# Kernel optimization log

Measured on AMD Instinct MI355X. Metric: run time of the kernel, lower is better.

The kernel has to match this reference:

```python
import jax, jax.numpy as jnp
import numpy as np

LVALS = [0, 1, 2]
IN_MULT = 128
OUT_MULT = 128
NREPS = len(LVALS)                      # 3 irreps
DIM = sum(2 * l + 1 for l in LVALS)     # 9 = 1 + 3 + 5
BATCH = 65536


def setup_inputs() -> dict:
    key = jax.random.key(0)
    k1, k2, k3 = jax.random.split(key, 3)
    f = jax.random.normal(k1, (BATCH, IN_MULT, DIM), dtype=jnp.float32)
    # xavier_uniform over (nreps*out_mult, in_mult): fan_out = nreps*out_mult, fan_in = in_mult
    limit = float(np.sqrt(6.0 / (IN_MULT + NREPS * OUT_MULT)))
    weight = jax.random.uniform(k2, (NREPS * OUT_MULT, IN_MULT), minval=-limit, maxval=limit, dtype=jnp.float32)
    bias = jax.random.normal(k3, (OUT_MULT, 1), dtype=jnp.float32) * 0.01
    # per-dim irrep index: [0, 1,1,1, 2,2,2,2,2]
    indices = jnp.asarray(np.repeat(np.arange(NREPS), [2 * l + 1 for l in LVALS]), dtype=jnp.int32)
    scalar_locs = jnp.asarray([0], dtype=jnp.int32)  # degree-0 column(s)
    return {"f": f, "weight": weight, "bias": bias, "indices": indices, "scalar_locs": scalar_locs}


def reference(f, weight, bias, indices, scalar_locs):
    # Torch does (weight @ f) -> (..., nreps*out_mult, dim), views to
    # (..., nreps, out_mult, dim), then gathers along the nreps axis with the
    # per-dim irrep index. Equivalently: use the per-dim weight slice directly,
    # avoiding the nreps-expanded intermediate.
    w3 = weight.reshape(NREPS, OUT_MULT, IN_MULT)
    wd = w3[indices]                              # (DIM, OUT_MULT, IN_MULT)
    out = jnp.einsum('dnm,bmd->bnd', wd, f)       # (B, OUT_MULT, DIM)
    # bias (+ identity activation) on scalar (degree-0) columns only
    scal = out[..., scalar_locs] + bias           # (B, OUT_MULT, nscalar)
    out = out.at[..., scalar_locs].set(scal)
    return out
```

## Files before the change

kernel.cpp:

```cpp
#include <hip/hip_runtime.h>


#define IN_MULT   128
#define OUT_MULT  128
#define DIM       9
#define TB        16
#define TPB       8
#define THREADS   256
#define ROWSTRIDE 136
#define NROWS     144

typedef __attribute__((ext_vector_type(8))) short short8;
typedef __attribute__((ext_vector_type(4))) float f32x4;

__device__ __forceinline__ unsigned short f2bf(float x) {
    unsigned u = __builtin_bit_cast(unsigned, x);
    u += 0x7FFFu + ((u >> 16) & 1u);
    return (unsigned short)(u >> 16);
}

__global__ __launch_bounds__(THREADS, 2)
void eqlin_kernel(const float* __restrict__ f,
                  const float* __restrict__ weight,
                  const float* __restrict__ bias,
                  float* __restrict__ out) {
    __shared__ unsigned short smem[NROWS * ROWSTRIDE];

    const int tid  = threadIdx.x;
    const int lane = tid & 63;
    const int wv   = tid >> 6;
    const int quad = lane >> 4;
    const int l16  = lane & 15;

    short8 bfrag[3][2][4];
    #pragma unroll
    for (int g = 0; g < 3; ++g)
        #pragma unroll
        for (int nf = 0; nf < 2; ++nf)
            #pragma unroll
            for (int kk = 0; kk < 4; ++kk) {
                const float* wp = weight
                    + (size_t)(g * OUT_MULT + wv * 32 + nf * 16 + l16) * IN_MULT
                    + kk * 32 + quad * 8;
                float4 u0 = *(const float4*)wp;
                float4 u1 = *(const float4*)(wp + 4);
                short8 bb;
                bb[0] = (short)f2bf(u0.x); bb[1] = (short)f2bf(u0.y);
                bb[2] = (short)f2bf(u0.z); bb[3] = (short)f2bf(u0.w);
                bb[4] = (short)f2bf(u1.x); bb[5] = (short)f2bf(u1.y);
                bb[6] = (short)f2bf(u1.z); bb[7] = (short)f2bf(u1.w);
                bfrag[g][nf][kk] = bb;
            }

    float biasv[2];
    #pragma unroll
    for (int nf = 0; nf < 2; ++nf)
        biasv[nf] = bias[wv * 32 + nf * 16 + l16];

    for (int it = 0; it < TPB; ++it) {
        const int b0 = (blockIdx.x * TPB + it) * TB;
        const float* ftile = f + (size_t)b0 * (IN_MULT * DIM);

        __syncthreads();

        #pragma unroll
        for (int rr = 0; rr < 18; rr += 6) {
            float4 v[6];
            #pragma unroll
            for (int q = 0; q < 6; ++q)
                v[q] = *(const float4*)(ftile + 4 * (tid + THREADS * (rr + q)));
            #pragma unroll
            for (int q = 0; q < 6; ++q) {
                const int F0  = 4 * (tid + THREADS * (rr + q));
                const int bl  = F0 / 1152;
                const int rem = F0 - bl * 1152;
                const int m0  = rem / 9;
                const int d0  = rem - m0 * 9;
                float vals[4] = {v[q].x, v[q].y, v[q].z, v[q].w};
                #pragma unroll
                for (int j = 0; j < 4; ++j) {
                    int dd = d0 + j, mm = m0;
                    if (dd >= 9) { dd -= 9; mm += 1; }
                    int row;
                    if (dd == 0)      row = bl;
                    else if (dd < 4)  row = 16 + bl * 3 + (dd - 1);
                    else              row = 64 + bl * 5 + (dd - 4);
                    smem[row * ROWSTRIDE + mm] = f2bf(vals[j]);
                }
            }
        }

        __syncthreads();

        #pragma unroll
        for (int mf = 0; mf < 9; ++mf) {
            const int g = (mf == 0) ? 0 : (mf < 4 ? 1 : 2);
            short8 a[4];
            #pragma unroll
            for (int kk = 0; kk < 4; ++kk)
                a[kk] = *(const short8*)&smem[(mf * 16 + l16) * ROWSTRIDE + kk * 32 + quad * 8];
            #pragma unroll
            for (int nf = 0; nf < 2; ++nf) {
                f32x4 acc = {0.f, 0.f, 0.f, 0.f};
                #pragma unroll
                for (int kk = 0; kk < 4; ++kk)
                    acc = __builtin_amdgcn_mfma_f32_16x16x32_bf16(a[kk], bfrag[g][nf][kk], acc, 0, 0, 0);
                if (g == 0) {
                    acc[0] += biasv[nf]; acc[1] += biasv[nf];
                    acc[2] += biasv[nf]; acc[3] += biasv[nf];
                }
                const int n = wv * 32 + nf * 16 + l16;
                #pragma unroll
                for (int reg = 0; reg < 4; ++reg) {
                    const int row = mf * 16 + quad * 4 + reg;
                    int bl, d;
                    if (mf == 0)      { bl = row; d = 0; }
                    else if (mf < 4)  { int r = row - 16; bl = r / 3; d = 1 + (r - 3 * bl); }
                    else              { int r = row - 64; bl = r / 5; d = 4 + (r - 5 * bl); }
                    out[(size_t)(b0 + bl) * (OUT_MULT * DIM) + n * DIM + d] = acc[reg];
                }
            }
        }
    }
}

extern "C" void kernel_launch(void* const* d_in, const int* in_sizes, int n_in,
                              void* d_out, int out_size, void* d_ws, size_t ws_size,
                              hipStream_t stream) {
    (void)n_in; (void)out_size; (void)d_ws; (void)ws_size;
    const float* f  = (const float*)d_in[0];
    const float* w  = (const float*)d_in[1];
    const float* bi = (const float*)d_in[2];
    float* out = (float*)d_out;

    const int batch   = in_sizes[0] / (IN_MULT * DIM);
    const int nblocks = batch / (TB * TPB);
    eqlin_kernel<<<nblocks, THREADS, 0, stream>>>(f, w, bi, out);
}
```

Before: 737.1 us.

## Stage output tile through shared memory for coalesced float4 global stores

Holds all MFMA accumulators in registers, then writes each half of the batch tile (8 rows) into the reused LDS buffer with an XOR swizzle. Afterwards it streams the staged data out with contiguous float4 stores. This replaces the scattered per-element global stores, which had stride DIM, and is meant to cut write transactions on a store-bound kernel. The cost is extra syncthreads, LDS traffic and about 72 more accumulator registers, which may reduce occupancy under launch_bounds(256,2).

```diff
diff --git a/kernel.cpp b/kernel.cpp
--- a/kernel.cpp
+++ b/kernel.cpp
@@ -9,6 +9,9 @@
 #define THREADS   256
 #define ROWSTRIDE 136
 #define NROWS     144
+#define ROWLEN    (OUT_MULT * DIM)
+#define HALF_B    8
+#define HALF_FLOATS (HALF_B * ROWLEN)
 
 typedef __attribute__((ext_vector_type(8))) short short8;
 typedef __attribute__((ext_vector_type(4))) float f32x4;
@@ -24,7 +27,9 @@
                   const float* __restrict__ weight,
                   const float* __restrict__ bias,
                   float* __restrict__ out) {
-    __shared__ unsigned short smem[NROWS * ROWSTRIDE];
+    __shared__ __align__(16) unsigned char smem_raw[NROWS * ROWSTRIDE * 2];
+    unsigned short* smem  = (unsigned short*)smem_raw;
+    float*          outsm = (float*)smem_raw;
 
     const int tid  = threadIdx.x;
     const int lane = tid & 63;
@@ -92,6 +97,7 @@
 
         __syncthreads();
 
+        f32x4 acc[9][2];
         #pragma unroll
         for (int mf = 0; mf < 9; ++mf) {
             const int g = (mf == 0) ? 0 : (mf < 4 ? 1 : 2);
@@ -101,24 +107,51 @@
                 a[kk] = *(const short8*)&smem[(mf * 16 + l16) * ROWSTRIDE + kk * 32 + quad * 8];
             #pragma unroll
             for (int nf = 0; nf < 2; ++nf) {
-                f32x4 acc = {0.f, 0.f, 0.f, 0.f};
+                f32x4 c = {0.f, 0.f, 0.f, 0.f};
                 #pragma unroll
                 for (int kk = 0; kk < 4; ++kk)
-                    acc = __builtin_amdgcn_mfma_f32_16x16x32_bf16(a[kk], bfrag[g][nf][kk], acc, 0, 0, 0);
+                    c = __builtin_amdgcn_mfma_f32_16x16x32_bf16(a[kk], bfrag[g][nf][kk], c, 0, 0, 0);
                 if (g == 0) {
-                    acc[0] += biasv[nf]; acc[1] += biasv[nf];
-                    acc[2] += biasv[nf]; acc[3] += biasv[nf];
+                    c[0] += biasv[nf]; c[1] += biasv[nf];
+                    c[2] += biasv[nf]; c[3] += biasv[nf];
                 }
-                const int n = wv * 32 + nf * 16 + l16;
+                acc[mf][nf] = c;
+            }
+        }
+
+        for (int h = 0; h < 2; ++h) {
+            __syncthreads();
+
+            #pragma unroll
+            for (int mf = 0; mf < 9; ++mf)
                 #pragma unroll
-                for (int reg = 0; reg < 4; ++reg) {
-                    const int row = mf * 16 + quad * 4 + reg;
-                    int bl, d;
-                    if (mf == 0)      { bl = row; d = 0; }
-                    else if (mf < 4)  { int r = row - 16; bl = r / 3; d = 1 + (r - 3 * bl); }
-                    else              { int r = row - 64; bl = r / 5; d = 4 + (r - 5 * bl); }
-                    out[(size_t)(b0 + bl) * (OUT_MULT * DIM) + n * DIM + d] = acc[reg];
+                for (int nf = 0; nf < 2; ++nf) {
+                    const int n = wv * 32 + nf * 16 + l16;
+                    #pragma unroll
+                    for (int reg = 0; reg < 4; ++reg) {
+                        const int row = mf * 16 + quad * 4 + reg;
+                        int bl, d;
+                        if (mf == 0)      { bl = row; d = 0; }
+                        else if (mf < 4)  { int r = row - 16; bl = r / 3; d = 1 + (r - 3 * bl); }
+                        else              { int r = row - 64; bl = r / 5; d = 4 + (r - 5 * bl); }
+                        if ((bl >> 3) == h) {
+                            const int blh = bl & 7;
+                            int idx = blh * ROWLEN + n * DIM + d;
+                            idx ^= (blh & 3) << 3;
+                            outsm[idx] = acc[mf][nf][reg];
+                        }
+                    }
                 }
+
+            __syncthreads();
+
+            float* op = out + (size_t)(b0 + h * HALF_B) * ROWLEN;
+            #pragma unroll
+            for (int r = 0; r < 9; ++r) {
+                const int c0   = 4 * (tid + THREADS * r);
+                const int blh  = c0 / ROWLEN;
+                const int pidx = c0 ^ ((blh & 3) << 3);
+                *(float4*)(op + c0) = *(const float4*)&outsm[pidx];
             }
         }
     }
```

Result: faster. 629.8 us (-14.6%).
